# Optimization experiments

Hardware: AMD Instinct MI355X
Metric: run time of the kernel (lower is better)

## Reference

```python
import jax, jax.numpy as jnp
import numpy as np
import math

HID = 1024
SLOTS = 64
KD = 32
B = 16384


def _normalize(v):
    # matches torch F.normalize(dim=-1, eps=1e-12)
    return v / jnp.clip(jnp.linalg.norm(v, axis=-1, keepdims=True), 1e-12)


def setup_inputs() -> dict:
    key = jax.random.key(0)
    ks = jax.random.split(key, 10)
    sc = lambda k, shape, s: jax.random.normal(k, shape, dtype=jnp.float32) * s
    return {
        "x": jax.random.normal(ks[0], (B, HID), dtype=jnp.float32),
        "key_w": sc(ks[1], (KD, HID), 0.02),
        "out_w": sc(ks[2], (HID, 2 * HID), 0.02),
        "out_b": jnp.zeros((HID,), jnp.float32),
        "gate_w": sc(ks[3], (HID, 2 * HID), 0.02),
        "gate_b": jnp.zeros((HID,), jnp.float32),
        "ln_g": jnp.ones((HID,), jnp.float32),
        "ln_b": jnp.zeros((HID,), jnp.float32),
        "pos_table": sc(ks[4], (SLOTS, KD), 1.0),
        "mem_keys": sc(ks[5], (SLOTS, KD), 0.02),
        "mem_vals": sc(ks[6], (SLOTS, HID), 0.5),
        "mem_age": jax.random.uniform(ks[7], (SLOTS,), dtype=jnp.float32) * 300.0,
        "mem_conf": jax.random.uniform(ks[8], (SLOTS,), dtype=jnp.float32),
        "slot_order": jnp.arange(SLOTS, dtype=jnp.int32),
    }


def reference(x, key_w, out_w, out_b, gate_w, gate_b, ln_g, ln_b,
              pos_table, mem_keys, mem_vals, mem_age, mem_conf, slot_order):
    # key projection  [B, KD]
    qk = x @ key_w.T
    # positional embedding of slot order, added to memory keys
    pos_emb = pos_table[slot_order % SLOTS]            # [S, KD]
    keys_with_pos = _normalize(mem_keys + 0.1 * pos_emb)
    query_norm = _normalize(qk)
    sim = (query_norm @ keys_with_pos.T) / math.sqrt(KD)  # [B, S]

    # multi-term salience (SalienceScorer.score with type_weight=0.8)
    recency = jnp.exp(-mem_age / 200.0)                # [S]
    freq = jnp.clip(mem_age, 1.0)                      # age.clamp(min=1) used as frequency
    freq_norm = jnp.log(freq + 1.0) / (jnp.log(freq.max() + 2.0) + 1e-8)
    bias = 0.2 * recency + 0.15 * freq_norm + 0.1 * mem_conf + 0.1 * 0.8  # [S]
    sal = jnp.clip(0.45 * sim + bias[None, :], 0.0, 1.0)

    attn = jax.nn.softmax(sal, axis=-1)                # [B, S]
    retrieved = attn @ mem_vals                        # [B, HID]

    combined = jnp.concatenate([x, retrieved], axis=-1)  # [B, 2*HID]
    gate_val = jax.nn.sigmoid(combined @ gate_w.T + gate_b)
    blended = gate_val * retrieved + (1.0 - gate_val) * x
    h = jax.nn.gelu(combined @ out_w.T + out_b, approximate=False)  # eval: dropout is identity
    y = h + blended

    # LayerNorm (eps=1e-5)
    mu = y.mean(axis=-1, keepdims=True)
    var = ((y - mu) ** 2).mean(axis=-1, keepdims=True)
    return (y - mu) / jnp.sqrt(var + 1e-5) * ln_g + ln_b
```

## Files before the change

kernel.cpp:

```cpp
#include <hip/hip_runtime.h>
#include <hip/hip_bf16.h>
#include <math.h>


typedef float    f32x4 __attribute__((ext_vector_type(4)));
typedef short    s16x8 __attribute__((ext_vector_type(8)));
typedef unsigned short u16;
typedef unsigned short u16x8 __attribute__((ext_vector_type(8)));

#define MFMA_BF16(a,b,c) __builtin_amdgcn_mfma_f32_16x16x32_bf16((a),(b),(c),0,0,0)

__device__ __forceinline__ void async16(void* lds, const void* g) {
  __builtin_amdgcn_global_load_lds((const __attribute__((address_space(1))) void*)g,
                                   (__attribute__((address_space(3))) void*)lds, 16, 0, 0);
}

__device__ __forceinline__ u16 f2bf(float f) {
  unsigned u = __float_as_uint(f);
  u += 0x7fffu + ((u >> 16) & 1u);
  return (u16)(u >> 16);
}
__device__ __forceinline__ float bf2f(u16 h) {
  return __uint_as_float(((unsigned)h) << 16);
}
__device__ __forceinline__ int ocol_of(int p) { return ((p >> 5) << 4) + (p & 15); }

__global__ __launch_bounds__(256) void k_prep(
    const float* __restrict__ mem_keys, const float* __restrict__ pos_table,
    const int* __restrict__ slot_order, const float* __restrict__ mem_age,
    const float* __restrict__ mem_conf, const float* __restrict__ key_w,
    const float* __restrict__ mem_vals, const float* __restrict__ gate_w,
    const float* __restrict__ out_w,
    float* __restrict__ kwp, float* __restrict__ biasv,
    u16* __restrict__ Wk, u16* __restrict__ Vcat, u16* __restrict__ Wcat) {
  const int b = blockIdx.x, tid = threadIdx.x;

  if (b == 0) {
    if (tid < 64) {
      int s = tid;
      float age  = mem_age[s];
      float freq = fmaxf(age, 1.0f);
      float fm = freq;
      #pragma unroll
      for (int o = 32; o; o >>= 1) fm = fmaxf(fm, __shfl_xor(fm, o));
      float freq_norm = logf(freq + 1.0f) / (logf(fm + 2.0f) + 1e-8f);
      float recency = expf(-age * (1.0f/200.0f));
      biasv[s] = 0.2f*recency + 0.15f*freq_norm + 0.1f*mem_conf[s] + 0.08f;

      int idx = slot_order[s] & 63;
      float k[32]; float ss = 0.f;
      #pragma unroll
      for (int d = 0; d < 32; d++) {
        float v = mem_keys[s*32+d] + 0.1f*pos_table[idx*32+d];
        k[d] = v; ss += v*v;
      }
      float inv = 1.0f / fmaxf(sqrtf(ss), 1e-12f);
      #pragma unroll
      for (int d = 0; d < 32; d++) kwp[s*33+d] = k[d]*inv;
    }
    for (int g = tid; g < 8192; g += 256) {
      float4 v = ((const float4*)key_w)[g];
      ushort4 o; o.x=f2bf(v.x); o.y=f2bf(v.y); o.z=f2bf(v.z); o.w=f2bf(v.w);
      *(ushort4*)(Wk + (size_t)g*4) = o;
    }
    return;
  }

  if (b <= 64) {
    int p0 = (b-1) * 32;
    for (int e = tid; e < 32*64; e += 256) {
      int pl = e >> 6, s = e & 63;
      int p = p0 + pl;
      Vcat[(size_t)p*64 + s] = f2bf(mem_vals[(size_t)s*1024 + ocol_of(p)]);
    }
    return;
  }

  __shared__ __align__(16) u16 sW[64*80];
  __shared__ __align__(16) u16 sV[64*80];
  const int pb = (b-65) * 64;
  const int lane = tid & 63, w = tid >> 6;
  const int ln15 = lane & 15, hi = lane >> 4;
  f32x4 acc[4];
  #pragma unroll
  for (int n = 0; n < 4; n++) acc[n] = {0.f,0.f,0.f,0.f};

  for (int kt = 0; kt < 16; ++kt) {
    #pragma unroll
    for (int j = 0; j < 4; j++) {
      int idx = tid + j*256;
      int row = idx >> 4, g4 = idx & 15;
      int p = pb + row;
      const float* wsrc = ((p >> 4) & 1) ? out_w : gate_w;
      float4 v = *(const float4*)&wsrc[(size_t)ocol_of(p)*2048 + 1024 + kt*64 + g4*4];
      ushort4 o; o.x=f2bf(v.x); o.y=f2bf(v.y); o.z=f2bf(v.z); o.w=f2bf(v.w);
      *(ushort4*)&sW[row*80 + g4*4] = o;
      float4 u = *(const float4*)&mem_vals[(size_t)row*1024 + kt*64 + g4*4];
      ushort4 p2; p2.x=f2bf(u.x); p2.y=f2bf(u.y); p2.z=f2bf(u.z); p2.w=f2bf(u.w);
      *(ushort4*)&sV[row*80 + g4*4] = p2;
    }
    __syncthreads();
    #pragma unroll
    for (int kk = 0; kk < 2; kk++) {
      int kb = kk*32 + hi*8;
      s16x8 a = *(const s16x8*)&sW[(w*16 + ln15)*80 + kb];
      #pragma unroll
      for (int n = 0; n < 4; n++) {
        s16x8 bv = *(const s16x8*)&sV[(n*16 + ln15)*80 + kb];
        acc[n] = MFMA_BF16(a, bv, acc[n]);
      }
    }
    __syncthreads();
  }
  #pragma unroll
  for (int n = 0; n < 4; n++)
    #pragma unroll
    for (int i = 0; i < 4; i++) {
      int p = pb + w*16 + hi*4 + i;
      Wcat[(size_t)p*1088 + 1024 + n*16 + ln15] = f2bf(acc[n][i]);
    }
}

__global__ __launch_bounds__(256) void k_front(
    const float* __restrict__ x, const float* __restrict__ gate_w,
    const float* __restrict__ out_w, const u16* __restrict__ Wk,
    const float* __restrict__ kwp, const float* __restrict__ biasv,
    u16* __restrict__ A, u16* __restrict__ Wcat) {
  const int b = blockIdx.x, tid = threadIdx.x;
  if (b >= 256) {
    for (int g = (b-256)*256 + tid; g < 524288; g += 32*256) {
      float4 v; int t, pb;
      if (g < 262144) { t = g;          v = *(const float4*)&gate_w[(size_t)(t>>8)*2048 + (t&255)*4]; pb = 0; }
      else            { t = g - 262144; v = *(const float4*)&out_w [(size_t)(t>>8)*2048 + (t&255)*4]; pb = 16; }
      int row = t >> 8, grp = t & 255;
      int p = ((row>>4)<<5) + pb + (row&15);
      ushort4 o; o.x=f2bf(v.x); o.y=f2bf(v.y); o.z=f2bf(v.z); o.w=f2bf(v.w);
      *(ushort4*)(Wcat + ((size_t)p*1088 + grp*4)) = o;
    }
    return;
  }

  __shared__ __align__(16) u16 sX[64*72];
  __shared__ float sQK[64*33];
  __shared__ float sK[64*33];
  __shared__ float sBias[64];
  __shared__ float sQn[64*32];

  const int lane = tid & 63, w = tid >> 6;
  const int ln15 = lane & 15, hi = lane >> 4;
  const size_t r0 = (size_t)b * 64;

  for (int i = tid; i < 64*33; i += 256) sK[i] = kwp[i];
  if (tid < 64) sBias[tid] = biasv[tid];

  f32x4 acc0 = {0.f,0.f,0.f,0.f}, acc1 = {0.f,0.f,0.f,0.f};
  const int xrow = tid >> 4, xc4 = tid & 15;
  for (int k0 = 0; k0 < 1024; k0 += 64) {
    #pragma unroll
    for (int j = 0; j < 4; j++) {
      int row = xrow + j*16;
      float4 v = *(const float4*)&x[(r0+row)*1024 + k0 + xc4*4];
      ushort4 o; o.x=f2bf(v.x); o.y=f2bf(v.y); o.z=f2bf(v.z); o.w=f2bf(v.w);
      *(ushort4*)&sX[row*72 + xc4*4] = o;
      *(ushort4*)&A[(r0+row)*1088 + k0 + xc4*4] = o;
    }
    __syncthreads();
    #pragma unroll
    for (int kk = 0; kk < 2; kk++) {
      int kb = kk*32 + hi*8;
      s16x8 a  = *(const s16x8*)&sX[(w*16 + ln15)*72 + kb];
      s16x8 b0 = *(const s16x8*)&Wk[(size_t)ln15*1024 + k0 + kb];
      s16x8 b1 = *(const s16x8*)&Wk[(size_t)(16+ln15)*1024 + k0 + kb];
      acc0 = MFMA_BF16(a, b0, acc0);
      acc1 = MFMA_BF16(a, b1, acc1);
    }
    __syncthreads();
  }
  #pragma unroll
  for (int i = 0; i < 4; i++) {
    sQK[(w*16 + hi*4 + i)*33 + ln15]      = acc0[i];
    sQK[(w*16 + hi*4 + i)*33 + 16 + ln15] = acc1[i];
  }
  __syncthreads();

  int d = lane & 31;
  for (int j = 0; j < 16; j++) {
    int rl = w*16 + j;
    float v = sQK[rl*33 + d];
    float sq = v*v;
    #pragma unroll
    for (int o = 16; o; o >>= 1) sq += __shfl_xor(sq, o);
    float qn = v / fmaxf(sqrtf(sq), 1e-12f);
    if (lane < 32) sQn[rl*32 + d] = qn;
    float accs = 0.f;
    #pragma unroll
    for (int dd = 0; dd < 32; dd++) accs += sK[lane*33+dd] * sQn[rl*32+dd];
    float sim = accs * 0.17677669529663687f;
    float sal = fminf(fmaxf(0.45f*sim + sBias[lane], 0.0f), 1.0f);
    float mx = sal;
    #pragma unroll
    for (int o = 32; o; o >>= 1) mx = fmaxf(mx, __shfl_xor(mx, o));
    float e = expf(sal - mx);
    float sm = e;
    #pragma unroll
    for (int o = 32; o; o >>= 1) sm += __shfl_xor(sm, o);
    A[(r0 + rl)*1088 + 1024 + lane] = f2bf(e / sm);
  }
}

__global__ __launch_bounds__(1024, 2) void k_gemm(
    const u16* __restrict__ A, const u16* __restrict__ Wcat,
    const u16* __restrict__ Vcat, const float* __restrict__ out_b,
    const float* __restrict__ gate_b, float* __restrict__ y) {
  __shared__ __align__(16) u16 sA[16384];
  __shared__ __align__(16) u16 sB[16384];

  const int tid = threadIdx.x, lane = tid & 63, w = tid >> 6;
  const int ln15 = lane & 15, hi = lane >> 4, p7 = ln15 & 7;
  const int wm = w >> 2, wn = w & 3;

  const int colblk = blockIdx.x & 7;
  const int rowblk = blockIdx.x >> 3;
  const size_t r0 = (size_t)rowblk * 256;
  const size_t c0 = (size_t)colblk * 256;

  const u16* gA = A    + r0 * 1088;
  const u16* gB = Wcat + c0 * 1088;
  const u16* gV = Vcat + c0 * 64;

  int offA[2], offB[2], offV[2];
  #pragma unroll
  for (int j = 0; j < 2; j++) {
    int c = tid + j*1024, row = c >> 3, pc = c & 7;
    int sw = ((pc ^ (row & 7)) << 3);
    offA[j] = row*1088 + sw;
    offB[j] = row*1088 + sw;
    offV[j] = row*64   + sw;
  }

  const int ck0 = (hi ^ p7) * 8;
  const int ck1 = ((4 | hi) ^ p7) * 8;
  const int arow = (wm*64 + ln15) * 64;
  const int brow = (wn*64 + ln15) * 64;

  f32x4 acc[4][4], accr[4][2];
  #pragma unroll
  for (int m = 0; m < 4; m++) {
    #pragma unroll
    for (int n = 0; n < 4; n++) acc[m][n] = {0.f, 0.f, 0.f, 0.f};
    accr[m][0] = {0.f,0.f,0.f,0.f}; accr[m][1] = {0.f,0.f,0.f,0.f};
  }

  #pragma unroll 1
  for (int kt = 0; kt < 17; ++kt) {
    const int ko = kt * 64;
    #pragma unroll
    for (int j = 0; j < 2; j++) {
      async16(&sA[(tid + j*1024)*8], gA + offA[j] + ko);
      async16(&sB[(tid + j*1024)*8], gB + offB[j] + ko);
    }
    __syncthreads();
    #pragma unroll
    for (int kk = 0; kk < 2; kk++) {
      const int ck = kk ? ck1 : ck0;
      s16x8 af[4], bfr[4];
      #pragma unroll
      for (int m = 0; m < 4; m++) af[m]  = *(const s16x8*)&sA[arow + m*1024 + ck];
      #pragma unroll
      for (int n = 0; n < 4; n++) bfr[n] = *(const s16x8*)&sB[brow + n*1024 + ck];
      #pragma unroll
      for (int m = 0; m < 4; m++)
        #pragma unroll
        for (int n = 0; n < 4; n++)
          acc[m][n] = MFMA_BF16(af[m], bfr[n], acc[m][n]);
    }
    __syncthreads();
  }

  #pragma unroll
  for (int j = 0; j < 2; j++) async16(&sB[(tid + j*1024)*8], gV + offV[j]);
  __syncthreads();
  #pragma unroll
  for (int kk = 0; kk < 2; kk++) {
    const int ck = kk ? ck1 : ck0;
    s16x8 af[4], bf0, bf1;
    #pragma unroll
    for (int m = 0; m < 4; m++) af[m] = *(const s16x8*)&sA[arow + m*1024 + ck];
    bf0 = *(const s16x8*)&sB[brow + ck];
    bf1 = *(const s16x8*)&sB[brow + 2*1024 + ck];
    #pragma unroll
    for (int m = 0; m < 4; m++) {
      accr[m][0] = MFMA_BF16(af[m], bf0, accr[m][0]);
      accr[m][1] = MFMA_BF16(af[m], bf1, accr[m][1]);
    }
  }

  #pragma unroll
  for (int s = 0; s < 2; s++) {
    int ocol = colblk*128 + wn*32 + s*16 + ln15;
    float gbv = gate_b[ocol], obv = out_b[ocol];
    #pragma unroll
    for (int m = 0; m < 4; m++) {
      #pragma unroll
      for (int i = 0; i < 4; i++) {
        size_t r = r0 + wm*64 + m*16 + hi*4 + i;
        float gg = acc[m][s*2+0][i] + gbv;
        float go = acc[m][s*2+1][i] + obv;
        float h  = 0.5f*go*(1.0f + erff(go*0.70710678118654752f));
        float sg = 1.0f/(1.0f + __expf(-gg));
        float rv = accr[m][s][i];
        float xv = bf2f(A[r*1088 + ocol]);
        y[r*1024 + ocol] = h + sg*rv + (1.0f - sg)*xv;
      }
    }
  }
}

__global__ __launch_bounds__(256) void k_ln(float* __restrict__ y, const float* __restrict__ g,
                                            const float* __restrict__ b) {
  int row  = blockIdx.x*4 + (threadIdx.x >> 6);
  int lane = threadIdx.x & 63;
  float4* p = (float4*)(y + (size_t)row*1024);
  float4 v[4];
  #pragma unroll
  for (int i = 0; i < 4; i++) v[i] = p[lane + 64*i];
  float s = 0.f;
  #pragma unroll
  for (int i = 0; i < 4; i++) s += v[i].x + v[i].y + v[i].z + v[i].w;
  #pragma unroll
  for (int o = 32; o; o >>= 1) s += __shfl_xor(s, o);
  float mu = s * (1.0f/1024.0f);
  float vs = 0.f;
  #pragma unroll
  for (int i = 0; i < 4; i++) {
    float d0 = v[i].x-mu, d1 = v[i].y-mu, d2 = v[i].z-mu, d3 = v[i].w-mu;
    vs += d0*d0 + d1*d1 + d2*d2 + d3*d3;
  }
  #pragma unroll
  for (int o = 32; o; o >>= 1) vs += __shfl_xor(vs, o);
  float inv = 1.0f / sqrtf(vs*(1.0f/1024.0f) + 1e-5f);
  const float4* gp = (const float4*)g;
  const float4* bp = (const float4*)b;
  #pragma unroll
  for (int i = 0; i < 4; i++) {
    float4 gv = gp[lane+64*i], bv = bp[lane+64*i], o4;
    o4.x = (v[i].x-mu)*inv*gv.x + bv.x;
    o4.y = (v[i].y-mu)*inv*gv.y + bv.y;
    o4.z = (v[i].z-mu)*inv*gv.z + bv.z;
    o4.w = (v[i].w-mu)*inv*gv.w + bv.w;
    p[lane + 64*i] = o4;
  }
}

extern "C" void kernel_launch(void* const* d_in, const int* in_sizes, int n_in,
                              void* d_out, int out_size, void* d_ws, size_t ws_size,
                              hipStream_t stream) {
  const float* x         = (const float*)d_in[0];
  const float* key_w     = (const float*)d_in[1];
  const float* out_w     = (const float*)d_in[2];
  const float* out_b     = (const float*)d_in[3];
  const float* gate_w    = (const float*)d_in[4];
  const float* gate_b    = (const float*)d_in[5];
  const float* ln_g      = (const float*)d_in[6];
  const float* ln_b      = (const float*)d_in[7];
  const float* pos_table = (const float*)d_in[8];
  const float* mem_keys  = (const float*)d_in[9];
  const float* mem_vals  = (const float*)d_in[10];
  const float* mem_age   = (const float*)d_in[11];
  const float* mem_conf  = (const float*)d_in[12];
  const int*   slot_order= (const int*)d_in[13];

  char* ws = (char*)d_ws;
  u16*   A    = (u16*)(ws + 0);
  u16*   Wcat = (u16*)(ws + 36700160);
  u16*   Vcat = (u16*)(ws + 41943040);
  u16*   Wk   = (u16*)(ws + 42205184);
  float* kwp  = (float*)(ws + 42270720);
  float* biasv= (float*)(ws + 42279168);
  float* y    = (float*)d_out;

  hipLaunchKernelGGL(k_prep,  dim3(97),   dim3(256),  0, stream,
                     mem_keys, pos_table, slot_order, mem_age, mem_conf,
                     key_w, mem_vals, gate_w, out_w, kwp, biasv, Wk, Vcat, Wcat);
  hipLaunchKernelGGL(k_front, dim3(288),  dim3(256),  0, stream,
                     x, gate_w, out_w, Wk, kwp, biasv, A, Wcat);
  hipLaunchKernelGGL(k_gemm,  dim3(512),  dim3(1024), 0, stream,
                     A, Wcat, Vcat, out_b, gate_b, y);
  hipLaunchKernelGGL(k_ln,    dim3(4096), dim3(256),  0, stream, y, ln_g, ln_b);
}
```

Before: 188.0 us.

## Fold prep kernel into front kernel and store pre-LayerNorm output as bf16

```diff
diff --git a/kernel.cpp b/kernel.cpp
--- a/kernel.cpp
+++ b/kernel.cpp
@@ -25,115 +25,73 @@
 }
 __device__ __forceinline__ int ocol_of(int p) { return ((p >> 5) << 4) + (p & 15); }
 
-__global__ __launch_bounds__(256) void k_prep(
-    const float* __restrict__ mem_keys, const float* __restrict__ pos_table,
-    const int* __restrict__ slot_order, const float* __restrict__ mem_age,
-    const float* __restrict__ mem_conf, const float* __restrict__ key_w,
-    const float* __restrict__ mem_vals, const float* __restrict__ gate_w,
-    const float* __restrict__ out_w,
-    float* __restrict__ kwp, float* __restrict__ biasv,
-    u16* __restrict__ Wk, u16* __restrict__ Vcat, u16* __restrict__ Wcat) {
-  const int b = blockIdx.x, tid = threadIdx.x;
-
-  if (b == 0) {
-    if (tid < 64) {
-      int s = tid;
-      float age  = mem_age[s];
-      float freq = fmaxf(age, 1.0f);
-      float fm = freq;
-      #pragma unroll
-      for (int o = 32; o; o >>= 1) fm = fmaxf(fm, __shfl_xor(fm, o));
-      float freq_norm = logf(freq + 1.0f) / (logf(fm + 2.0f) + 1e-8f);
-      float recency = expf(-age * (1.0f/200.0f));
-      biasv[s] = 0.2f*recency + 0.15f*freq_norm + 0.1f*mem_conf[s] + 0.08f;
-
-      int idx = slot_order[s] & 63;
-      float k[32]; float ss = 0.f;
-      #pragma unroll
-      for (int d = 0; d < 32; d++) {
-        float v = mem_keys[s*32+d] + 0.1f*pos_table[idx*32+d];
-        k[d] = v; ss += v*v;
-      }
-      float inv = 1.0f / fmaxf(sqrtf(ss), 1e-12f);
-      #pragma unroll
-      for (int d = 0; d < 32; d++) kwp[s*33+d] = k[d]*inv;
-    }
-    for (int g = tid; g < 8192; g += 256) {
-      float4 v = ((const float4*)key_w)[g];
-      ushort4 o; o.x=f2bf(v.x); o.y=f2bf(v.y); o.z=f2bf(v.z); o.w=f2bf(v.w);
-      *(ushort4*)(Wk + (size_t)g*4) = o;
-    }
-    return;
-  }
-
-  if (b <= 64) {
-    int p0 = (b-1) * 32;
-    for (int e = tid; e < 32*64; e += 256) {
-      int pl = e >> 6, s = e & 63;
-      int p = p0 + pl;
-      Vcat[(size_t)p*64 + s] = f2bf(mem_vals[(size_t)s*1024 + ocol_of(p)]);
-    }
-    return;
-  }
-
-  __shared__ __align__(16) u16 sW[64*80];
-  __shared__ __align__(16) u16 sV[64*80];
-  const int pb = (b-65) * 64;
-  const int lane = tid & 63, w = tid >> 6;
-  const int ln15 = lane & 15, hi = lane >> 4;
-  f32x4 acc[4];
-  #pragma unroll
-  for (int n = 0; n < 4; n++) acc[n] = {0.f,0.f,0.f,0.f};
-
-  for (int kt = 0; kt < 16; ++kt) {
-    #pragma unroll
-    for (int j = 0; j < 4; j++) {
-      int idx = tid + j*256;
-      int row = idx >> 4, g4 = idx & 15;
-      int p = pb + row;
-      const float* wsrc = ((p >> 4) & 1) ? out_w : gate_w;
-      float4 v = *(const float4*)&wsrc[(size_t)ocol_of(p)*2048 + 1024 + kt*64 + g4*4];
-      ushort4 o; o.x=f2bf(v.x); o.y=f2bf(v.y); o.z=f2bf(v.z); o.w=f2bf(v.w);
-      *(ushort4*)&sW[row*80 + g4*4] = o;
-      float4 u = *(const float4*)&mem_vals[(size_t)row*1024 + kt*64 + g4*4];
-      ushort4 p2; p2.x=f2bf(u.x); p2.y=f2bf(u.y); p2.z=f2bf(u.z); p2.w=f2bf(u.w);
-      *(ushort4*)&sV[row*80 + g4*4] = p2;
-    }
-    __syncthreads();
-    #pragma unroll
-    for (int kk = 0; kk < 2; kk++) {
-      int kb = kk*32 + hi*8;
-      s16x8 a = *(const s16x8*)&sW[(w*16 + ln15)*80 + kb];
-      #pragma unroll
-      for (int n = 0; n < 4; n++) {
-        s16x8 bv = *(const s16x8*)&sV[(n*16 + ln15)*80 + kb];
-        acc[n] = MFMA_BF16(a, bv, acc[n]);
-      }
-    }
-    __syncthreads();
-  }
-  #pragma unroll
-  for (int n = 0; n < 4; n++)
-    #pragma unroll
-    for (int i = 0; i < 4; i++) {
-      int p = pb + w*16 + hi*4 + i;
-      Wcat[(size_t)p*1088 + 1024 + n*16 + ln15] = f2bf(acc[n][i]);
-    }
-}
-
 __global__ __launch_bounds__(256) void k_front(
     const float* __restrict__ x, const float* __restrict__ gate_w,
-    const float* __restrict__ out_w, const u16* __restrict__ Wk,
-    const float* __restrict__ kwp, const float* __restrict__ biasv,
-    u16* __restrict__ A, u16* __restrict__ Wcat) {
+    const float* __restrict__ out_w, const float* __restrict__ key_w,
+    const float* __restrict__ mem_vals, const float* __restrict__ mem_keys,
+    const float* __restrict__ pos_table, const int* __restrict__ slot_order,
+    const float* __restrict__ mem_age, const float* __restrict__ mem_conf,
+    u16* __restrict__ A, u16* __restrict__ Wcat, u16* __restrict__ Vcat) {
   const int b = blockIdx.x, tid = threadIdx.x;
+
+  if (b >= 288) {
+    const int pb = (b - 288) * 64;
+    for (int e = tid; e < 64*64; e += 256) {
+      int pl = e >> 6, s = e & 63;
+      int p = pb + pl;
+      Vcat[(size_t)p*64 + s] = f2bf(mem_vals[(size_t)s*1024 + ocol_of(p)]);
+    }
+    __shared__ __align__(16) u16 sW[64*80];
+    __shared__ __align__(16) u16 sV[64*80];
+    const int lane = tid & 63, w = tid >> 6;
+    const int ln15 = lane & 15, hi = lane >> 4;
+    f32x4 acc[4];
+    #pragma unroll
+    for (int n = 0; n < 4; n++) acc[n] = {0.f,0.f,0.f,0.f};
+    for (int kt = 0; kt < 16; ++kt) {
+      #pragma unroll
+      for (int j = 0; j < 4; j++) {
+        int idx = tid + j*256;
+        int row = idx >> 4, g4 = idx & 15;
+        int p = pb + row;
+        const float* wsrc = ((p >> 4) & 1) ? out_w : gate_w;
+        float4 v = *(const float4*)&wsrc[(size_t)ocol_of(p)*2048 + 1024 + kt*64 + g4*4];
+        ushort4 o; o.x=f2bf(v.x); o.y=f2bf(v.y); o.z=f2bf(v.z); o.w=f2bf(v.w);
+        *(ushort4*)&sW[row*80 + g4*4] = o;
+        float4 u = *(const float4*)&mem_vals[(size_t)row*1024 + kt*64 + g4*4];
+        ushort4 p2; p2.x=f2bf(u.x); p2.y=f2bf(u.y); p2.z=f2bf(u.z); p2.w=f2bf(u.w);
+        *(ushort4*)&sV[row*80 + g4*4] = p2;
+      }
+      __syncthreads();
+      #pragma unroll
+      for (int kk = 0; kk < 2; kk++) {
+        int kb = kk*32 + hi*8;
+        s16x8 a = *(const s16x8*)&sW[(w*16 + ln15)*80 + kb];
+        #pragma unroll
+        for (int n = 0; n < 4; n++) {
+          s16x8 bv = *(const s16x8*)&sV[(n*16 + ln15)*80 + kb];
+          acc[n] = MFMA_BF16(a, bv, acc[n]);
+        }
+      }
+      __syncthreads();
+    }
+    #pragma unroll
+    for (int n = 0; n < 4; n++)
+      #pragma unroll
+      for (int i = 0; i < 4; i++) {
+        int p = pb + w*16 + hi*4 + i;
+        Wcat[(size_t)p*1088 + 1024 + n*16 + ln15] = f2bf(acc[n][i]);
+      }
+    return;
+  }
+
   if (b >= 256) {
     for (int g = (b-256)*256 + tid; g < 524288; g += 32*256) {
-      float4 v; int t, pb;
-      if (g < 262144) { t = g;          v = *(const float4*)&gate_w[(size_t)(t>>8)*2048 + (t&255)*4]; pb = 0; }
-      else            { t = g - 262144; v = *(const float4*)&out_w [(size_t)(t>>8)*2048 + (t&255)*4]; pb = 16; }
+      float4 v; int t, pb2;
+      if (g < 262144) { t = g;          v = *(const float4*)&gate_w[(size_t)(t>>8)*2048 + (t&255)*4]; pb2 = 0; }
+      else            { t = g - 262144; v = *(const float4*)&out_w [(size_t)(t>>8)*2048 + (t&255)*4]; pb2 = 16; }
       int row = t >> 8, grp = t & 255;
-      int p = ((row>>4)<<5) + pb + (row&15);
+      int p = ((row>>4)<<5) + pb2 + (row&15);
       ushort4 o; o.x=f2bf(v.x); o.y=f2bf(v.y); o.z=f2bf(v.z); o.w=f2bf(v.w);
       *(ushort4*)(Wcat + ((size_t)p*1088 + grp*4)) = o;
     }
@@ -141,6 +99,7 @@
   }
 
   __shared__ __align__(16) u16 sX[64*72];
+  __shared__ __align__(16) u16 sWk[32*72];
   __shared__ float sQK[64*33];
   __shared__ float sK[64*33];
   __shared__ float sBias[64];
@@ -150,8 +109,28 @@
   const int ln15 = lane & 15, hi = lane >> 4;
   const size_t r0 = (size_t)b * 64;
 
-  for (int i = tid; i < 64*33; i += 256) sK[i] = kwp[i];
-  if (tid < 64) sBias[tid] = biasv[tid];
+  if (tid < 64) {
+    int s = tid;
+    float age  = mem_age[s];
+    float freq = fmaxf(age, 1.0f);
+    float fm = freq;
+    #pragma unroll
+    for (int o = 32; o; o >>= 1) fm = fmaxf(fm, __shfl_xor(fm, o));
+    float freq_norm = logf(freq + 1.0f) / (logf(fm + 2.0f) + 1e-8f);
+    float recency = expf(-age * (1.0f/200.0f));
+    sBias[s] = 0.2f*recency + 0.15f*freq_norm + 0.1f*mem_conf[s] + 0.08f;
+
+    int idx = slot_order[s] & 63;
+    float k[32]; float ss = 0.f;
+    #pragma unroll
+    for (int d = 0; d < 32; d++) {
+      float v = mem_keys[s*32+d] + 0.1f*pos_table[idx*32+d];
+      k[d] = v; ss += v*v;
+    }
+    float inv = 1.0f / fmaxf(sqrtf(ss), 1e-12f);
+    #pragma unroll
+    for (int d = 0; d < 32; d++) sK[s*33+d] = k[d]*inv;
+  }
 
   f32x4 acc0 = {0.f,0.f,0.f,0.f}, acc1 = {0.f,0.f,0.f,0.f};
   const int xrow = tid >> 4, xc4 = tid & 15;
@@ -164,13 +143,21 @@
       *(ushort4*)&sX[row*72 + xc4*4] = o;
       *(ushort4*)&A[(r0+row)*1088 + k0 + xc4*4] = o;
     }
+    #pragma unroll
+    for (int j = 0; j < 2; j++) {
+      int idx = tid + j*256;
+      int row = idx >> 4, c4 = idx & 15;
+      float4 v = *(const float4*)&key_w[(size_t)row*1024 + k0 + c4*4];
+      ushort4 o; o.x=f2bf(v.x); o.y=f2bf(v.y); o.z=f2bf(v.z); o.w=f2bf(v.w);
+      *(ushort4*)&sWk[row*72 + c4*4] = o;
+    }
     __syncthreads();
     #pragma unroll
     for (int kk = 0; kk < 2; kk++) {
       int kb = kk*32 + hi*8;
       s16x8 a  = *(const s16x8*)&sX[(w*16 + ln15)*72 + kb];
-      s16x8 b0 = *(const s16x8*)&Wk[(size_t)ln15*1024 + k0 + kb];
-      s16x8 b1 = *(const s16x8*)&Wk[(size_t)(16+ln15)*1024 + k0 + kb];
+      s16x8 b0 = *(const s16x8*)&sWk[ln15*72 + kb];
+      s16x8 b1 = *(const s16x8*)&sWk[(16+ln15)*72 + kb];
       acc0 = MFMA_BF16(a, b0, acc0);
       acc1 = MFMA_BF16(a, b1, acc1);
     }
@@ -211,7 +198,7 @@
 __global__ __launch_bounds__(1024, 2) void k_gemm(
     const u16* __restrict__ A, const u16* __restrict__ Wcat,
     const u16* __restrict__ Vcat, const float* __restrict__ out_b,
-    const float* __restrict__ gate_b, float* __restrict__ y) {
+    const float* __restrict__ gate_b, u16* __restrict__ yb) {
   __shared__ __align__(16) u16 sA[16384];
   __shared__ __align__(16) u16 sB[16384];
 
@@ -310,45 +297,47 @@
         float sg = 1.0f/(1.0f + __expf(-gg));
         float rv = accr[m][s][i];
         float xv = bf2f(A[r*1088 + ocol]);
-        y[r*1024 + ocol] = h + sg*rv + (1.0f - sg)*xv;
+        yb[r*1024 + ocol] = f2bf(h + sg*rv + (1.0f - sg)*xv);
       }
     }
   }
 }
 
-__global__ __launch_bounds__(256) void k_ln(float* __restrict__ y, const float* __restrict__ g,
-                                            const float* __restrict__ b) {
+__global__ __launch_bounds__(256) void k_ln(const u16* __restrict__ yb,
+                                            const float* __restrict__ g,
+                                            const float* __restrict__ b,
+                                            float* __restrict__ out) {
   int row  = blockIdx.x*4 + (threadIdx.x >> 6);
   int lane = threadIdx.x & 63;
-  float4* p = (float4*)(y + (size_t)row*1024);
-  float4 v[4];
-  #pragma unroll
-  for (int i = 0; i < 4; i++) v[i] = p[lane + 64*i];
+  const u16* p = yb + (size_t)row*1024 + lane*16;
+  u16x8 h0 = *(const u16x8*)p;
+  u16x8 h1 = *(const u16x8*)(p + 8);
+  float v[16];
+  #pragma unroll
+  for (int i = 0; i < 8; i++) { v[i] = bf2f((u16)h0[i]); v[8+i] = bf2f((u16)h1[i]); }
   float s = 0.f;
   #pragma unroll
-  for (int i = 0; i < 4; i++) s += v[i].x + v[i].y + v[i].z + v[i].w;
+  for (int i = 0; i < 16; i++) s += v[i];
   #pragma unroll
   for (int o = 32; o; o >>= 1) s += __shfl_xor(s, o);
   float mu = s * (1.0f/1024.0f);
   float vs = 0.f;
   #pragma unroll
-  for (int i = 0; i < 4; i++) {
-    float d0 = v[i].x-mu, d1 = v[i].y-mu, d2 = v[i].z-mu, d3 = v[i].w-mu;
-    vs += d0*d0 + d1*d1 + d2*d2 + d3*d3;
-  }
+  for (int i = 0; i < 16; i++) { float d0 = v[i]-mu; vs += d0*d0; }
   #pragma unroll
   for (int o = 32; o; o >>= 1) vs += __shfl_xor(vs, o);
   float inv = 1.0f / sqrtf(vs*(1.0f/1024.0f) + 1e-5f);
-  const float4* gp = (const float4*)g;
-  const float4* bp = (const float4*)b;
+  const float4* gp = (const float4*)(g + lane*16);
+  const float4* bp = (const float4*)(b + lane*16);
+  float4* op = (float4*)(out + (size_t)row*1024 + lane*16);
   #pragma unroll
   for (int i = 0; i < 4; i++) {
-    float4 gv = gp[lane+64*i], bv = bp[lane+64*i], o4;
-    o4.x = (v[i].x-mu)*inv*gv.x + bv.x;
-    o4.y = (v[i].y-mu)*inv*gv.y + bv.y;
-    o4.z = (v[i].z-mu)*inv*gv.z + bv.z;
-    o4.w = (v[i].w-mu)*inv*gv.w + bv.w;
-    p[lane + 64*i] = o4;
+    float4 gv = gp[i], bv = bp[i], o4;
+    o4.x = (v[i*4+0]-mu)*inv*gv.x + bv.x;
+    o4.y = (v[i*4+1]-mu)*inv*gv.y + bv.y;
+    o4.z = (v[i*4+2]-mu)*inv*gv.z + bv.z;
+    o4.w = (v[i*4+3]-mu)*inv*gv.w + bv.w;
+    op[i] = o4;
   }
 }
 
@@ -374,17 +363,14 @@
   u16*   A    = (u16*)(ws + 0);
   u16*   Wcat = (u16*)(ws + 36700160);
   u16*   Vcat = (u16*)(ws + 41943040);
-  u16*   Wk   = (u16*)(ws + 42205184);
-  float* kwp  = (float*)(ws + 42270720);
-  float* biasv= (float*)(ws + 42279168);
+  u16*   yb   = (u16*)(ws + 42205184);
   float* y    = (float*)d_out;
 
-  hipLaunchKernelGGL(k_prep,  dim3(97),   dim3(256),  0, stream,
-                     mem_keys, pos_table, slot_order, mem_age, mem_conf,
-                     key_w, mem_vals, gate_w, out_w, kwp, biasv, Wk, Vcat, Wcat);
-  hipLaunchKernelGGL(k_front, dim3(288),  dim3(256),  0, stream,
-                     x, gate_w, out_w, Wk, kwp, biasv, A, Wcat);
+  hipLaunchKernelGGL(k_front, dim3(320),  dim3(256),  0, stream,
+                     x, gate_w, out_w, key_w, mem_vals, mem_keys, pos_table,
+                     slot_order, mem_age, mem_conf, A, Wcat, Vcat);
   hipLaunchKernelGGL(k_gemm,  dim3(512),  dim3(1024), 0, stream,
-                     A, Wcat, Vcat, out_b, gate_b, y);
-  hipLaunchKernelGGL(k_ln,    dim3(4096), dim3(256),  0, stream, y, ln_g, ln_b);
-}
+                     A, Wcat, Vcat, out_b, gate_b, yb);
+  hipLaunchKernelGGL(k_ln,    dim3(4096), dim3(256),  0, stream,
+                     yb, ln_g, ln_b, y);
+}
```

Result: faster. 174.7 us (-7.1%).
